# Performance work log

Hardware: AMD Instinct MI355X
Metric: run time of the kernel (lower is better)

Reference implementation:

```python
import math
import jax, jax.numpy as jnp
import numpy as np

B, S, D, QK, H = 4, 4096, 1024, 128, 2048  # hidden = int(2.0 * dim)
NUM_BUCKETS, MAX_DIST = 32, 128
LN_EPS = 1e-5


def setup_inputs() -> dict:
    key = jax.random.key(0)
    ks = jax.random.split(key, 7)
    x = jax.random.normal(ks[0], (B, S, D), jnp.float32)
    ln_g = jnp.ones((D,), jnp.float32)
    ln_b = jnp.zeros((D,), jnp.float32)
    Wh = jax.random.normal(ks[1], (D, 2 * H), jnp.float32) * 0.02
    bh = jnp.zeros((2 * H,), jnp.float32)
    Wqk = jax.random.normal(ks[2], (D, QK), jnp.float32) * 0.02
    bqk = jnp.zeros((QK,), jnp.float32)
    os_gamma = jax.random.normal(ks[3], (2, QK), jnp.float32) * 0.02  # nn.init.normal_(std=0.02)
    os_beta = jnp.zeros((2, QK), jnp.float32)
    Wo = jax.random.normal(ks[4], (H, D), jnp.float32) * 0.02
    bo = jnp.zeros((D,), jnp.float32)
    rel_emb = jax.random.normal(ks[5], (NUM_BUCKETS, 1), jnp.float32) * 0.02
    return {"x": x, "ln_g": ln_g, "ln_b": ln_b, "Wh": Wh, "bh": bh,
            "Wqk": Wqk, "bqk": bqk, "os_gamma": os_gamma, "os_beta": os_beta,
            "Wo": Wo, "bo": bo, "rel_emb": rel_emb}


def _t5_rel_bias(rel_emb, seq_len, scale):
    # non-causal T5 relative position bucket (num_buckets halved to 16)
    pos = jnp.arange(seq_len)
    rel = pos[None, :] - pos[:, None]  # k_pos - q_pos -> [i, j]
    n = -rel
    nb = NUM_BUCKETS // 2  # 16
    me = nb // 2           # max_exact = 8
    ret = (n < 0).astype(jnp.int32) * nb
    na = jnp.abs(n)
    val_large = me + (jnp.log(jnp.maximum(na, 1).astype(jnp.float32) / me)
                      / math.log(MAX_DIST / me) * (nb - me)).astype(jnp.int32)
    val_large = jnp.minimum(val_large, nb - 1)
    bucket = ret + jnp.where(na < me, na, val_large)  # [S, S] in [0, 31]
    return rel_emb[bucket, 0] * scale  # [S, S]


def reference(x, ln_g, ln_b, Wh, bh, Wqk, bqk, os_gamma, os_beta, Wo, bo, rel_emb):
    seq_len = x.shape[-2]
    # LayerNorm
    mu = jnp.mean(x, axis=-1, keepdims=True)
    var = jnp.mean(jnp.square(x - mu), axis=-1, keepdims=True)
    normed = (x - mu) * jax.lax.rsqrt(var + LN_EPS) * ln_g + ln_b
    # hidden (v, gate) with SiLU
    hidden = jax.nn.silu(normed @ Wh + bh)  # [B, S, 2H]
    v, gate = hidden[..., :H], hidden[..., H:]
    # qk projection + offset/scale into q, k
    qk = jax.nn.silu(normed @ Wqk + bqk)  # [B, S, QK]
    q = qk * os_gamma[0] + os_beta[0]
    k = qk * os_gamma[1] + os_beta[1]
    sim = jnp.einsum('bid,bjd->bij', q, k)  # [B, S, S]
    sim = sim + _t5_rel_bias(rel_emb, seq_len, float(D) ** 0.5)
    attn = jnp.square(jax.nn.relu(sim / seq_len))  # ReLU^2, no softmax
    out = jnp.einsum('bij,bjd->bid', attn, v) * gate  # [B, S, H]
    out = out @ Wo + bo
    return out + x  # add_residual
```

## Files before the change

### kernel.cpp

```cpp
#include <hip/hip_runtime.h>
#include <hip/hip_bf16.h>
#include <math.h>

typedef __bf16 bf16_t;
typedef __bf16 bf16x8 __attribute__((ext_vector_type(8)));
typedef __bf16 bf16x4 __attribute__((ext_vector_type(4)));
typedef float  f32x4  __attribute__((ext_vector_type(4)));
typedef int    i32x4  __attribute__((ext_vector_type(4)));

#define S_LEN 4096
#define D_DIM 1024
#define QK_DIM 128
#define H_DIM 2048
#define BATCH 4

__device__ __forceinline__ void gld_lds16(const void* g, void* l) {
  __builtin_amdgcn_global_load_lds((const __attribute__((address_space(1))) void*)g,
                                   (__attribute__((address_space(3))) void*)l, 16, 0, 0);
}

__device__ __forceinline__ float silu_f(float v) {
  return v / (1.0f + __expf(-v));
}

__device__ __forceinline__ bf16x8 as_bf(i32x4 v) {
  union { i32x4 a; bf16x8 b; } u; u.a = v; return u.b;
}

__device__ __forceinline__ float ldf(const void* p, size_t i, int f32) {
  return f32 ? ((const float*)p)[i] : (float)((const bf16_t*)p)[i];
}

__global__ void probe_k(const unsigned* __restrict__ ln_g_raw, int* __restrict__ flag) {
  if (threadIdx.x == 0) flag[0] = (ln_g_raw[0] == 0x3F800000u) ? 1 : 0;
}

#define M_HID 0
#define M_QK 1
#define M_SCORE 2
#define M_PV 3
#define M_OUT 4

template <int MODE, int K, int KS>
__global__ __launch_bounds__(512, (KS == 64 ? 2 : 4))
void gemm4(const bf16_t* __restrict__ A, const bf16_t* __restrict__ Bt,
           const void* e0, const void* e1, const float* __restrict__ ef,
           void* o0, void* o1, const int* __restrict__ dflag)
{
  constexpr int NT   = K / KS;
  constexpr int NSL  = KS / 32;
  constexpr int ASLOT = 128 * KS * 2;
  constexpr int BSLOT = 256 * KS * 2;
  constexpr int RA   = ASLOT / 8192;
  constexpr int RB   = BSLOT / 8192;
  constexpr int SLD  = RA + RB;
  constexpr int MR   = 4;
  constexpr int RWB  = KS * 2;

  __shared__ __align__(16) char lds[3 * (ASLOT + BSLOT)];

  const int t = threadIdx.x;
  const int w = t >> 6, lane = t & 63;
  const int quad = lane >> 4, col = lane & 15;
  const int wm = (w >> 2) * 64;
  const int wn = (w & 3) * 64;

  const int gx = gridDim.x;
  const int nwg = gx * (int)gridDim.y;
  const int orig = (int)blockIdx.y * gx + (int)blockIdx.x;
  const int wg = (orig & 7) * (nwg >> 3) + (orig >> 3);
  const int bx = wg & (gx - 1), by = wg >> __builtin_ctz(gx);
  const int m0 = bx * 128, n0 = by * 256;

  const bf16_t* const Ap = A + (size_t)m0 * K;
  const bf16_t* const Bp = Bt + (size_t)n0 * K;

  size_t aoff[RA], boff[RB];
#pragma unroll
  for (int c = 0; c < RA; ++c) {
    const int P = c * 8192 + t * 16;
    const int L = P ^ (((P >> 7) & (NSL == 1 ? 3 : 7)) << 4);
    aoff[c] = (size_t)(L / RWB) * K + ((L & (RWB - 1)) >> 1);
  }
#pragma unroll
  for (int c = 0; c < RB; ++c) {
    const int P = c * 8192 + t * 16;
    const int L = P ^ (((P >> 7) & (NSL == 1 ? 3 : 7)) << 4);
    boff[c] = (size_t)(L / RWB) * K + ((L & (RWB - 1)) >> 1);
  }

  const int xr = (NSL == 1) ? ((quad ^ ((col >> 1) & 3)) << 4)
                            : ((quad ^ (col & 7)) << 4);
  const unsigned ldsI = (unsigned)(size_t)&lds[0];
  const unsigned aStat = ldsI + (unsigned)((wm + col) * RWB + xr);
  const unsigned bStat = ldsI + 3u * ASLOT + (unsigned)((wn + col) * RWB + xr);

  f32x4 acc[MR][4] = {};
  i32x4 aF[MR][NSL], bF[4][NSL];

#define SB() __builtin_amdgcn_sched_barrier(0)
#define BARR() do { SB(); __builtin_amdgcn_s_barrier(); SB(); } while (0)
#define DSR(dst, addr, lit) \
  asm volatile("ds_read_b128 %0, %1 offset:" #lit : "=v"(dst) : "v"(addr))
#define WL(n) asm volatile("s_waitcnt lgkmcnt(" #n ")" ::: "memory")
#define WAITV0() asm volatile("s_waitcnt vmcnt(0)" ::: "memory")
#define VWS() do {                                                             \
    if constexpr (SLD == 3) asm volatile("s_waitcnt vmcnt(3)" ::: "memory");   \
    else                    asm volatile("s_waitcnt vmcnt(6)" ::: "memory");   \
  } while (0)

#define MMI(mi, ni, kk)                                                        \
  acc[mi][ni] = __builtin_amdgcn_mfma_f32_16x16x32_bf16(                       \
      as_bf(aF[mi][kk]), as_bf(bF[ni][kk]), acc[mi][ni], 0, 0, 0)
#define MM4(ni, kk) do { MMI(0, ni, kk); MMI(1, ni, kk);                       \
                         MMI(2, ni, kk); MMI(3, ni, kk); } while (0)

#define STG(ts, sl) do {                                                       \
    char* da_ = (char*)lds + (sl) * ASLOT + t * 16;                            \
    char* db_ = (char*)lds + 3 * ASLOT + (sl) * BSLOT + t * 16;                \
    const bf16_t* ga_ = Ap + (size_t)(ts) * KS;                                \
    const bf16_t* gb_ = Bp + (size_t)(ts) * KS;                                \
    _Pragma("unroll") for (int c_ = 0; c_ < RA; ++c_)                          \
      gld_lds16(ga_ + aoff[c_], da_ + c_ * 8192);                              \
    _Pragma("unroll") for (int c_ = 0; c_ < RB; ++c_)                          \
      gld_lds16(gb_ + boff[c_], db_ + c_ * 8192);                              \
  } while (0)

  STG(0, 0);
  STG(1, 1);
  VWS();
  BARR();

  int bsel = 0, ssel = 2;
  for (int tt = 0; tt < NT; ++tt) {
    const unsigned aAd = aStat + (unsigned)(bsel * ASLOT);
    const unsigned bAd = bStat + (unsigned)(bsel * BSLOT);
    if constexpr (NSL == 1) {
      DSR(bF[0][0], bAd, 0);
      DSR(aF[0][0], aAd, 0);
      DSR(aF[1][0], aAd, 1024);
      DSR(aF[2][0], aAd, 2048);
      DSR(aF[3][0], aAd, 3072);
      DSR(bF[1][0], bAd, 1024);
      DSR(bF[2][0], bAd, 2048);
      DSR(bF[3][0], bAd, 3072);
      if (tt + 2 < NT) STG(tt + 2, ssel);
      __builtin_amdgcn_s_setprio(1);
      WL(6); SB(); MMI(0, 0, 0);
      WL(5); SB(); MMI(1, 0, 0);
      WL(4); SB(); MMI(2, 0, 0);
      WL(3); SB(); MMI(3, 0, 0);
      WL(2); SB(); MM4(1, 0);
      WL(1); SB(); MM4(2, 0);
      WL(0); SB(); MM4(3, 0);
      __builtin_amdgcn_s_setprio(0);
    } else {
      const unsigned aA1 = aAd ^ 64u, bA1 = bAd ^ 64u;
      DSR(bF[0][0], bAd, 0);
      DSR(aF[0][0], aAd, 0);
      DSR(aF[1][0], aAd, 2048);
      DSR(aF[2][0], aAd, 4096);
      DSR(aF[3][0], aAd, 6144);
      DSR(bF[1][0], bAd, 2048);
      DSR(bF[2][0], bAd, 4096);
      DSR(bF[3][0], bAd, 6144);
      DSR(bF[0][1], bA1, 0);
      DSR(aF[0][1], aA1, 0);
      DSR(aF[1][1], aA1, 2048);
      DSR(aF[2][1], aA1, 4096);
      DSR(aF[3][1], aA1, 6144);
      DSR(bF[1][1], bA1, 2048);
      DSR(bF[2][1], bA1, 4096);
      DSR(bF[3][1], bA1, 6144);
      if (tt + 2 < NT) STG(tt + 2, ssel);
      __builtin_amdgcn_s_setprio(1);
      WL(14); SB(); MMI(0, 0, 0);
      WL(13); SB(); MMI(1, 0, 0);
      WL(12); SB(); MMI(2, 0, 0);
      WL(11); SB(); MMI(3, 0, 0);
      WL(10); SB(); MM4(1, 0);
      WL(9);  SB(); MM4(2, 0);
      WL(8);  SB(); MM4(3, 0);
      WL(6);  SB(); MMI(0, 0, 1);
      WL(5);  SB(); MMI(1, 0, 1);
      WL(4);  SB(); MMI(2, 0, 1);
      WL(3);  SB(); MMI(3, 0, 1);
      WL(2);  SB(); MM4(1, 1);
      WL(1);  SB(); MM4(2, 1);
      WL(0);  SB(); MM4(3, 1);
      __builtin_amdgcn_s_setprio(0);
    }
    SB();
    if (tt + 1 < NT) {
      if (tt + 2 < NT) VWS();
      else WAITV0();
    }
    BARR();
    bsel = (bsel == 2) ? 0 : bsel + 1;
    ssel = (ssel == 2) ? 0 : ssel + 1;
  }

#undef SB
#undef BARR
#undef DSR
#undef WL
#undef WAITV0
#undef VWS
#undef MMI
#undef MM4
#undef STG

  __syncthreads();

  int f32 = 0;
  if constexpr (MODE == M_HID || MODE == M_OUT) f32 = dflag[0];

  if constexpr (MODE == M_OUT) {
    float (*swzf)[16][68] = (float (*)[16][68])lds;
#pragma unroll
    for (int m = 0; m < MR; ++m) {
      __syncthreads();
#pragma unroll
      for (int j = 0; j < 4; ++j)
#pragma unroll
        for (int r = 0; r < 4; ++r)
          swzf[w][quad * 4 + r][j * 16 + col] = acc[m][j][r];
      __syncthreads();
#pragma unroll
      for (int it = 0; it < 4; ++it) {
        const int task = it * 64 + lane, gr = task >> 4, ch = task & 15;
        const int gm = m0 + wm + m * 16 + gr;
        const int gnc = n0 + wn + ch * 4;
        f32x4 vv = *(const f32x4*)&swzf[w][gr][ch * 4];
        float xr4[4], r4[4];
        if (f32) {
          float4 t4 = *(const float4*)((const float*)e1 + (size_t)gm * D_DIM + gnc);
          xr4[0] = t4.x; xr4[1] = t4.y; xr4[2] = t4.z; xr4[3] = t4.w;
        } else {
          bf16x4 t4 = *(const bf16x4*)((const bf16_t*)e1 + (size_t)gm * D_DIM + gnc);
#pragma unroll
          for (int qq = 0; qq < 4; ++qq) xr4[qq] = (float)t4[qq];
        }
#pragma unroll
        for (int qq = 0; qq < 4; ++qq)
          r4[qq] = vv[qq] + ldf(e0, gnc + qq, f32) + xr4[qq];
        if (f32) {
          float4 s4 = {r4[0], r4[1], r4[2], r4[3]};
          *(float4*)((float*)o0 + (size_t)gm * D_DIM + gnc) = s4;
        } else {
          bf16x4 s4;
#pragma unroll
          for (int qq = 0; qq < 4; ++qq) s4[qq] = (bf16_t)r4[qq];
          *(bf16x4*)((bf16_t*)o0 + (size_t)gm * D_DIM + gnc) = s4;
        }
      }
    }
    return;
  }

  if constexpr (MODE == M_HID) {
    if (n0 < H_DIM) {
      bf16_t (*swzT)[16][72] = (bf16_t (*)[16][72])lds;
      const int bb  = m0 >> 12;
      const int smb = (m0 + wm) & (S_LEN - 1);
#pragma unroll
      for (int j = 0; j < 4; ++j) {
        __syncthreads();
        const int gnj = n0 + wn + j * 16;
        const float bhv = ldf(e0, gnj + col, f32);
#pragma unroll
        for (int m = 0; m < MR; ++m)
#pragma unroll
          for (int r = 0; r < 4; ++r)
            swzT[w][col][m * 16 + quad * 4 + r] = (bf16_t)silu_f(acc[m][j][r] + bhv);
        __syncthreads();
#pragma unroll
        for (int it = 0; it < 2; ++it) {
          const int task = it * 64 + lane, gr = task >> 3, ch = task & 7;
          bf16x8 vv = *(const bf16x8*)&swzT[w][gr][ch * 8];
          const size_t off = ((size_t)bb * H_DIM + (gnj + gr)) * S_LEN + smb + ch * 8;
          *(bf16x8*)((bf16_t*)o0 + off) = vv;
        }
      }
      return;
    }
  }

  if constexpr (MODE == M_HID || MODE == M_SCORE || MODE == M_PV) {
    bf16_t (*swzb)[16][72] = (bf16_t (*)[16][72])lds;
#pragma unroll
    for (int m = 0; m < MR; ++m) {
      __syncthreads();
#pragma unroll
      for (int j = 0; j < 4; ++j) {
        const int gn = n0 + wn + j * 16 + col;
#pragma unroll
        for (int r = 0; r < 4; ++r) {
          const float val = acc[m][j][r];
          bf16_t sv;
          if constexpr (MODE == M_HID) {
            sv = (bf16_t)silu_f(val + ldf(e0, gn, f32));
          } else if constexpr (MODE == M_SCORE) {
            const int gm = m0 + wm + m * 16 + quad * 4 + r;
            float wgt = fmaxf((val + ef[gm - gn + (S_LEN - 1)]) *
                              (1.0f / (float)S_LEN), 0.0f);
            sv = (bf16_t)(wgt * wgt);
          } else {
            sv = (bf16_t)val;
          }
          swzb[w][quad * 4 + r][j * 16 + col] = sv;
        }
      }
      __syncthreads();
#pragma unroll
      for (int it = 0; it < 2; ++it) {
        const int task = it * 64 + lane, gr = task >> 3, ch = task & 7;
        const int gm  = m0 + wm + m * 16 + gr;
        const int gnb = n0 + wn + ch * 8;
        bf16x8 vv = *(const bf16x8*)&swzb[w][gr][ch * 8];
        if constexpr (MODE == M_HID) {
          *(bf16x8*)((bf16_t*)o1 + (size_t)gm * H_DIM + (gnb - H_DIM)) = vv;
        } else if constexpr (MODE == M_SCORE) {
          *(bf16x8*)((bf16_t*)o0 + (size_t)gm * S_LEN + gnb) = vv;
        } else {
          bf16x8 g8 = *(const bf16x8*)((const bf16_t*)e0 + (size_t)gm * H_DIM + gnb);
          bf16x8 r8;
#pragma unroll
          for (int qq = 0; qq < 8; ++qq)
            r8[qq] = (bf16_t)((float)vv[qq] * (float)g8[qq]);
          *(bf16x8*)((bf16_t*)o0 + (size_t)gm * H_DIM + gnb) = r8;
        }
      }
    }
  }
}

template <int MODE>
__global__ __launch_bounds__(256)
void gemm_bt(const bf16_t* __restrict__ A, const bf16_t* __restrict__ Bt,
             int M, int N, int K,
             const void* e0, const void* e1, const void* e2,
             const float* __restrict__ ef,
             void* o0, void* o1, const int* __restrict__ dflag)
{
  __shared__ __align__(16) bf16_t As[128 * 32];
  __shared__ __align__(16) bf16_t Bs[128 * 32];
  const int t = threadIdx.x;
  const int w = t >> 6, lane = t & 63;
  const int quad = lane >> 4, col = lane & 15;
  const int wm = (w >> 1) << 6, wn = (w & 1) << 6;
  const int m0 = blockIdx.x * 128, n0 = blockIdx.y * 128;
  const int f32 = dflag[0];

  f32x4 acc[4][4] = {};

  for (int k0 = 0; k0 < K; k0 += 32) {
    __syncthreads();
    for (int p = 0; p < 2; ++p) {
      const int chunk = w * 2 + p;
      const int fl = (chunk * 64 + lane) * 8;
      const int r = fl >> 5, c = fl & 31;
      gld_lds16(A  + (size_t)(m0 + r) * K + (k0 + c), &As[chunk * 512]);
      gld_lds16(Bt + (size_t)(n0 + r) * K + (k0 + c), &Bs[chunk * 512]);
    }
    __syncthreads();

    bf16x8 af[4], bfr[4];
#pragma unroll
    for (int i = 0; i < 4; ++i)
      af[i] = *(const bf16x8*)&As[(wm + i * 16 + col) * 32 + quad * 8];
#pragma unroll
    for (int i = 0; i < 4; ++i)
      bfr[i] = *(const bf16x8*)&Bs[(wn + i * 16 + col) * 32 + quad * 8];
#pragma unroll
    for (int i = 0; i < 4; ++i)
#pragma unroll
      for (int j = 0; j < 4; ++j)
        acc[i][j] = __builtin_amdgcn_mfma_f32_16x16x32_bf16(af[i], bfr[j], acc[i][j], 0, 0, 0);
  }

#pragma unroll
  for (int i = 0; i < 4; ++i) {
#pragma unroll
    for (int j = 0; j < 4; ++j) {
#pragma unroll
      for (int r = 0; r < 4; ++r) {
        const int gm = m0 + wm + i * 16 + quad * 4 + r;
        const int gn = n0 + wn + j * 16 + col;
        float val = acc[i][j][r] + ldf(e0, gn, f32);
        float s = silu_f(val);
        ((bf16_t*)o0)[(size_t)gm * QK_DIM + gn] =
            (bf16_t)(s * ldf(e1, gn, f32) + ldf(e2, gn, f32));
        ((bf16_t*)o1)[(size_t)gm * QK_DIM + gn] =
            (bf16_t)(s * ldf(e1, QK_DIM + gn, f32) + ldf(e2, QK_DIM + gn, f32));
      }
    }
  }
}

__global__ __launch_bounds__(256)
void layernorm_k(const void* __restrict__ x, const void* __restrict__ g,
                 const void* __restrict__ be, bf16_t* __restrict__ out,
                 const int* __restrict__ dflag)
{
  const int row = blockIdx.x;
  const int t = threadIdx.x;
  const int f32 = dflag[0];
  float f[4];
  if (f32) {
    const float* xr = (const float*)x + (size_t)row * D_DIM;
    float4 xv = *(const float4*)&xr[t * 4];
    f[0] = xv.x; f[1] = xv.y; f[2] = xv.z; f[3] = xv.w;
  } else {
    const bf16_t* xr = (const bf16_t*)x + (size_t)row * D_DIM;
    bf16x4 xv = *(const bf16x4*)&xr[t * 4];
#pragma unroll
    for (int i = 0; i < 4; ++i) f[i] = (float)xv[i];
  }
  float s = 0.f, sq = 0.f;
#pragma unroll
  for (int i = 0; i < 4; ++i) { s += f[i]; sq += f[i] * f[i]; }
#pragma unroll
  for (int off = 32; off > 0; off >>= 1) {
    s += __shfl_down(s, off);
    sq += __shfl_down(sq, off);
  }
  __shared__ float red[8];
  const int w = t >> 6;
  if ((t & 63) == 0) { red[w] = s; red[4 + w] = sq; }
  __syncthreads();
  s = red[0] + red[1] + red[2] + red[3];
  sq = red[4] + red[5] + red[6] + red[7];
  const float mu = s * (1.0f / D_DIM);
  const float var = sq * (1.0f / D_DIM) - mu * mu;
  const float inv = rsqrtf(var + 1e-5f);
  bf16x4 ov;
#pragma unroll
  for (int i = 0; i < 4; ++i) {
    float nv = (f[i] - mu) * inv * ldf(g, t * 4 + i, f32) + ldf(be, t * 4 + i, f32);
    ov[i] = (bf16_t)nv;
  }
  *(bf16x4*)&out[(size_t)row * D_DIM + t * 4] = ov;
}

__global__ __launch_bounds__(256)
void transpose_k(const void* __restrict__ src, bf16_t* __restrict__ dst,
                 int R, int C, const int* __restrict__ dflag)
{
  __shared__ bf16_t tile[32][33];
  const int f32 = dflag[0];
  const int c0 = blockIdx.x * 32, r0 = blockIdx.y * 32;
  for (int i = threadIdx.y; i < 32; i += 8)
    tile[i][threadIdx.x] = (bf16_t)ldf(src, (size_t)(r0 + i) * C + (c0 + threadIdx.x), f32);
  __syncthreads();
  for (int i = threadIdx.y; i < 32; i += 8)
    dst[(size_t)(c0 + i) * R + (r0 + threadIdx.x)] = tile[threadIdx.x][i];
}

__global__ void bias_k(const void* __restrict__ rel_emb, float* __restrict__ bias,
                       const int* __restrict__ dflag)
{
  int d = blockIdx.x * 256 + threadIdx.x;
  if (d >= 2 * S_LEN - 1) return;
  const int f32 = dflag[0];
  int n = d - (S_LEN - 1);
  int ret = (n < 0) ? 16 : 0;
  int na = n < 0 ? -n : n;
  int b;
  if (na < 8) b = na;
  else {
    float vl = logf((float)na * (1.0f / 8.0f)) / logf(16.0f) * 8.0f;
    int vi = 8 + (int)vl;
    b = vi > 15 ? 15 : vi;
  }
  bias[d] = ldf(rel_emb, ret + b, f32) * 32.0f;
}

extern "C" void kernel_launch(void* const* d_in, const int* in_sizes, int n_in,
                              void* d_out, int out_size, void* d_ws, size_t ws_size,
                              hipStream_t stream)
{
  const void* x    = d_in[0];
  const void* ln_g = d_in[1];
  const void* ln_b = d_in[2];
  const void* Wh   = d_in[3];
  const void* bh   = d_in[4];
  const void* Wqk  = d_in[5];
  const void* bqk  = d_in[6];
  const void* osg  = d_in[7];
  const void* osb  = d_in[8];
  const void* Wo   = d_in[9];
  const void* bo   = d_in[10];
  const void* rel  = d_in[11];

  const int BS = BATCH * S_LEN;
  char* p = (char*)d_ws;
  int*    flags  = (int*)p;     p += 256;
  float*  bias   = (float*)p;   p += (size_t)8192 * 4;
  bf16_t* WhT    = (bf16_t*)p;  p += (size_t)4096 * 1024 * 2;
  bf16_t* WqkT   = (bf16_t*)p;  p += (size_t)128 * 1024 * 2;
  bf16_t* WoT    = (bf16_t*)p;  p += (size_t)1024 * 2048 * 2;
  bf16_t* q      = (bf16_t*)p;  p += (size_t)BS * QK_DIM * 2;
  bf16_t* kk     = (bf16_t*)p;  p += (size_t)BS * QK_DIM * 2;
  bf16_t* vT     = (bf16_t*)p;  p += (size_t)BS * H_DIM * 2;
  bf16_t* gate   = (bf16_t*)p;  p += (size_t)BS * H_DIM * 2;
  bf16_t* normed = (bf16_t*)p;  p += (size_t)BS * D_DIM * 2;
  bf16_t* attn   = normed;
  bf16_t* pvg    = gate;

  probe_k<<<1, 64, 0, stream>>>((const unsigned*)ln_g, flags);
  bias_k<<<32, 256, 0, stream>>>(rel, bias, flags);
  transpose_k<<<dim3(4096 / 32, 1024 / 32), dim3(32, 8), 0, stream>>>(Wh, WhT, 1024, 4096, flags);
  transpose_k<<<dim3(128 / 32, 1024 / 32), dim3(32, 8), 0, stream>>>(Wqk, WqkT, 1024, 128, flags);
  transpose_k<<<dim3(1024 / 32, 2048 / 32), dim3(32, 8), 0, stream>>>(Wo, WoT, 2048, 1024, flags);
  layernorm_k<<<BS, 256, 0, stream>>>(x, ln_g, ln_b, normed, flags);

  gemm4<M_HID, 1024, 32><<<dim3(BS / 128, 4096 / 256), 512, 0, stream>>>(
      normed, WhT, bh, nullptr, nullptr, vT, gate, flags);
  gemm_bt<M_QK><<<dim3(BS / 128, 1), 256, 0, stream>>>(
      normed, WqkT, BS, QK_DIM, 1024, bqk, osg, osb, nullptr, q, kk, flags);

  for (int b = 0; b < BATCH; ++b) {
    gemm4<M_SCORE, QK_DIM, 32><<<dim3(S_LEN / 128, S_LEN / 256), 512, 0, stream>>>(
        q + (size_t)b * S_LEN * QK_DIM, kk + (size_t)b * S_LEN * QK_DIM,
        nullptr, nullptr, bias, attn, nullptr, flags);
    gemm4<M_PV, S_LEN, 64><<<dim3(S_LEN / 128, H_DIM / 256), 512, 0, stream>>>(
        attn, vT + (size_t)b * S_LEN * H_DIM,
        gate + (size_t)b * S_LEN * H_DIM, nullptr, nullptr,
        pvg + (size_t)b * S_LEN * H_DIM, nullptr, flags);
  }

  gemm4<M_OUT, H_DIM, 32><<<dim3(BS / 128, 1024 / 256), 512, 0, stream>>>(
      pvg, WoT, bo, x, nullptr, d_out, nullptr, flags);
}
```

Baseline: 770.0 us.

## Load A operand directly from global into registers, bypassing LDS staging

Removes LDS staging for the A tile in the shared GEMM kernel; each wave now issues global_load_dwordx4 for its A fragments one k-step ahead into a register double buffer, while B stays on the LDS pipeline. This cuts LDS footprint and ds_read traffic for A. In exchange, A rows are fetched redundantly by multiple waves with less coalesced access, and register pressure rises from the extra fragment buffer.

```diff
diff --git a/kernel.cpp b/kernel.cpp
--- a/kernel.cpp
+++ b/kernel.cpp
@@ -43,21 +43,17 @@
 
 template <int MODE, int K, int KS>
 __global__ __launch_bounds__(512, (KS == 64 ? 2 : 4))
-void gemm4(const bf16_t* __restrict__ A, const bf16_t* __restrict__ Bt,
+void gemm5(const bf16_t* __restrict__ A, const bf16_t* __restrict__ Bt,
            const void* e0, const void* e1, const float* __restrict__ ef,
            void* o0, void* o1, const int* __restrict__ dflag)
 {
   constexpr int NT   = K / KS;
   constexpr int NSL  = KS / 32;
-  constexpr int ASLOT = 128 * KS * 2;
   constexpr int BSLOT = 256 * KS * 2;
-  constexpr int RA   = ASLOT / 8192;
   constexpr int RB   = BSLOT / 8192;
-  constexpr int SLD  = RA + RB;
-  constexpr int MR   = 4;
   constexpr int RWB  = KS * 2;
 
-  __shared__ __align__(16) char lds[3 * (ASLOT + BSLOT)];
+  __shared__ __align__(16) char lds[3 * BSLOT];
 
   const int t = threadIdx.x;
   const int w = t >> 6, lane = t & 63;
@@ -75,13 +71,7 @@
   const bf16_t* const Ap = A + (size_t)m0 * K;
   const bf16_t* const Bp = Bt + (size_t)n0 * K;
 
-  size_t aoff[RA], boff[RB];
-#pragma unroll
-  for (int c = 0; c < RA; ++c) {
-    const int P = c * 8192 + t * 16;
-    const int L = P ^ (((P >> 7) & (NSL == 1 ? 3 : 7)) << 4);
-    aoff[c] = (size_t)(L / RWB) * K + ((L & (RWB - 1)) >> 1);
-  }
+  size_t boff[RB];
 #pragma unroll
   for (int c = 0; c < RB; ++c) {
     const int P = c * 8192 + t * 16;
@@ -92,40 +82,61 @@
   const int xr = (NSL == 1) ? ((quad ^ ((col >> 1) & 3)) << 4)
                             : ((quad ^ (col & 7)) << 4);
   const unsigned ldsI = (unsigned)(size_t)&lds[0];
-  const unsigned aStat = ldsI + (unsigned)((wm + col) * RWB + xr);
-  const unsigned bStat = ldsI + 3u * ASLOT + (unsigned)((wn + col) * RWB + xr);
-
-  f32x4 acc[MR][4] = {};
-  i32x4 aF[MR][NSL], bF[4][NSL];
+  const unsigned bStat = ldsI + (unsigned)((wn + col) * RWB + xr);
+
+  unsigned voff[4];
+#pragma unroll
+  for (int mi = 0; mi < 4; ++mi)
+    voff[mi] = (unsigned)(((wm + mi * 16 + col) * (size_t)K + quad * 8) * 2);
+
+  f32x4 acc[4][4] = {};
+  i32x4 aCur[4][NSL], aNxt[4][NSL], bF[4][NSL];
 
 #define SB() __builtin_amdgcn_sched_barrier(0)
 #define BARR() do { SB(); __builtin_amdgcn_s_barrier(); SB(); } while (0)
 #define DSR(dst, addr, lit) \
   asm volatile("ds_read_b128 %0, %1 offset:" #lit : "=v"(dst) : "v"(addr))
+#define GLA(dst, off, lit) \
+  asm volatile("global_load_dwordx4 %0, %1, %2 offset:" #lit \
+               : "=v"(dst) : "v"(off), "s"(Ap))
 #define WL(n) asm volatile("s_waitcnt lgkmcnt(" #n ")" ::: "memory")
 #define WAITV0() asm volatile("s_waitcnt vmcnt(0)" ::: "memory")
 #define VWS() do {                                                             \
-    if constexpr (SLD == 3) asm volatile("s_waitcnt vmcnt(3)" ::: "memory");   \
-    else                    asm volatile("s_waitcnt vmcnt(6)" ::: "memory");   \
+    if constexpr (RB == 2) asm volatile("s_waitcnt vmcnt(2)" ::: "memory");    \
+    else                   asm volatile("s_waitcnt vmcnt(4)" ::: "memory");    \
+  } while (0)
+
+#define LDA(dst) do {                                                          \
+    _Pragma("unroll") for (int mi_ = 0; mi_ < 4; ++mi_) {                      \
+      GLA(dst[mi_][0], voff[mi_], 0);                                          \
+      if constexpr (NSL == 2) GLA(dst[mi_][1], voff[mi_], 64);                 \
+    }                                                                          \
+  } while (0)
+
+#define ACOPY() do {                                                           \
+    _Pragma("unroll") for (int mi_ = 0; mi_ < 4; ++mi_)                        \
+    _Pragma("unroll") for (int kk_ = 0; kk_ < NSL; ++kk_)                      \
+      aCur[mi_][kk_] = aNxt[mi_][kk_];                                         \
+    _Pragma("unroll") for (int mi_ = 0; mi_ < 4; ++mi_)                        \
+      voff[mi_] += KS * 2;                                                     \
   } while (0)
 
 #define MMI(mi, ni, kk)                                                        \
   acc[mi][ni] = __builtin_amdgcn_mfma_f32_16x16x32_bf16(                       \
-      as_bf(aF[mi][kk]), as_bf(bF[ni][kk]), acc[mi][ni], 0, 0, 0)
+      as_bf(aCur[mi][kk]), as_bf(bF[ni][kk]), acc[mi][ni], 0, 0, 0)
 #define MM4(ni, kk) do { MMI(0, ni, kk); MMI(1, ni, kk);                       \
                          MMI(2, ni, kk); MMI(3, ni, kk); } while (0)
 
 #define STG(ts, sl) do {                                                       \
-    char* da_ = (char*)lds + (sl) * ASLOT + t * 16;                            \
-    char* db_ = (char*)lds + 3 * ASLOT + (sl) * BSLOT + t * 16;                \
-    const bf16_t* ga_ = Ap + (size_t)(ts) * KS;                                \
+    char* db_ = (char*)lds + (sl) * BSLOT + t * 16;                            \
     const bf16_t* gb_ = Bp + (size_t)(ts) * KS;                                \
-    _Pragma("unroll") for (int c_ = 0; c_ < RA; ++c_)                          \
-      gld_lds16(ga_ + aoff[c_], da_ + c_ * 8192);                              \
     _Pragma("unroll") for (int c_ = 0; c_ < RB; ++c_)                          \
       gld_lds16(gb_ + boff[c_], db_ + c_ * 8192);                              \
   } while (0)
 
+  LDA(aCur);
+#pragma unroll
+  for (int mi = 0; mi < 4; ++mi) voff[mi] += KS * 2;
   STG(0, 0);
   STG(1, 1);
   VWS();
@@ -133,69 +144,49 @@
 
   int bsel = 0, ssel = 2;
   for (int tt = 0; tt < NT; ++tt) {
-    const unsigned aAd = aStat + (unsigned)(bsel * ASLOT);
     const unsigned bAd = bStat + (unsigned)(bsel * BSLOT);
     if constexpr (NSL == 1) {
       DSR(bF[0][0], bAd, 0);
-      DSR(aF[0][0], aAd, 0);
-      DSR(aF[1][0], aAd, 1024);
-      DSR(aF[2][0], aAd, 2048);
-      DSR(aF[3][0], aAd, 3072);
       DSR(bF[1][0], bAd, 1024);
       DSR(bF[2][0], bAd, 2048);
       DSR(bF[3][0], bAd, 3072);
-      if (tt + 2 < NT) STG(tt + 2, ssel);
-      __builtin_amdgcn_s_setprio(1);
-      WL(6); SB(); MMI(0, 0, 0);
-      WL(5); SB(); MMI(1, 0, 0);
-      WL(4); SB(); MMI(2, 0, 0);
-      WL(3); SB(); MMI(3, 0, 0);
-      WL(2); SB(); MM4(1, 0);
-      WL(1); SB(); MM4(2, 0);
-      WL(0); SB(); MM4(3, 0);
-      __builtin_amdgcn_s_setprio(0);
     } else {
-      const unsigned aA1 = aAd ^ 64u, bA1 = bAd ^ 64u;
+      const unsigned bA1 = bAd ^ 64u;
       DSR(bF[0][0], bAd, 0);
-      DSR(aF[0][0], aAd, 0);
-      DSR(aF[1][0], aAd, 2048);
-      DSR(aF[2][0], aAd, 4096);
-      DSR(aF[3][0], aAd, 6144);
       DSR(bF[1][0], bAd, 2048);
       DSR(bF[2][0], bAd, 4096);
       DSR(bF[3][0], bAd, 6144);
       DSR(bF[0][1], bA1, 0);
-      DSR(aF[0][1], aA1, 0);
-      DSR(aF[1][1], aA1, 2048);
-      DSR(aF[2][1], aA1, 4096);
-      DSR(aF[3][1], aA1, 6144);
       DSR(bF[1][1], bA1, 2048);
       DSR(bF[2][1], bA1, 4096);
       DSR(bF[3][1], bA1, 6144);
-      if (tt + 2 < NT) STG(tt + 2, ssel);
-      __builtin_amdgcn_s_setprio(1);
-      WL(14); SB(); MMI(0, 0, 0);
-      WL(13); SB(); MMI(1, 0, 0);
-      WL(12); SB(); MMI(2, 0, 0);
-      WL(11); SB(); MMI(3, 0, 0);
-      WL(10); SB(); MM4(1, 0);
-      WL(9);  SB(); MM4(2, 0);
-      WL(8);  SB(); MM4(3, 0);
-      WL(6);  SB(); MMI(0, 0, 1);
-      WL(5);  SB(); MMI(1, 0, 1);
-      WL(4);  SB(); MMI(2, 0, 1);
-      WL(3);  SB(); MMI(3, 0, 1);
-      WL(2);  SB(); MM4(1, 1);
-      WL(1);  SB(); MM4(2, 1);
-      WL(0);  SB(); MM4(3, 1);
-      __builtin_amdgcn_s_setprio(0);
-    }
+    }
+    if (tt + 1 < NT) LDA(aNxt);
+    if (tt + 2 < NT) STG(tt + 2, ssel);
+    __builtin_amdgcn_s_setprio(1);
+    if constexpr (NSL == 1) {
+      WL(3); SB(); MM4(0, 0);
+      WL(2); SB(); MM4(1, 0);
+      WL(1); SB(); MM4(2, 0);
+      WL(0); SB(); MM4(3, 0);
+    } else {
+      WL(7); SB(); MM4(0, 0);
+      WL(6); SB(); MM4(1, 0);
+      WL(5); SB(); MM4(2, 0);
+      WL(4); SB(); MM4(3, 0);
+      WL(3); SB(); MM4(0, 1);
+      WL(2); SB(); MM4(1, 1);
+      WL(1); SB(); MM4(2, 1);
+      WL(0); SB(); MM4(3, 1);
+    }
+    __builtin_amdgcn_s_setprio(0);
     SB();
     if (tt + 1 < NT) {
       if (tt + 2 < NT) VWS();
       else WAITV0();
     }
     BARR();
+    if (tt + 1 < NT) ACOPY();
     bsel = (bsel == 2) ? 0 : bsel + 1;
     ssel = (ssel == 2) ? 0 : ssel + 1;
   }
@@ -203,9 +194,12 @@
 #undef SB
 #undef BARR
 #undef DSR
+#undef GLA
 #undef WL
 #undef WAITV0
 #undef VWS
+#undef LDA
+#undef ACOPY
 #undef MMI
 #undef MM4
 #undef STG
@@ -218,7 +212,7 @@
   if constexpr (MODE == M_OUT) {
     float (*swzf)[16][68] = (float (*)[16][68])lds;
 #pragma unroll
-    for (int m = 0; m < MR; ++m) {
+    for (int m = 0; m < 4; ++m) {
       __syncthreads();
 #pragma unroll
       for (int j = 0; j < 4; ++j)
@@ -269,7 +263,7 @@
         const int gnj = n0 + wn + j * 16;
         const float bhv = ldf(e0, gnj + col, f32);
 #pragma unroll
-        for (int m = 0; m < MR; ++m)
+        for (int m = 0; m < 4; ++m)
 #pragma unroll
           for (int r = 0; r < 4; ++r)
             swzT[w][col][m * 16 + quad * 4 + r] = (bf16_t)silu_f(acc[m][j][r] + bhv);
@@ -289,7 +283,7 @@
   if constexpr (MODE == M_HID || MODE == M_SCORE || MODE == M_PV) {
     bf16_t (*swzb)[16][72] = (bf16_t (*)[16][72])lds;
 #pragma unroll
-    for (int m = 0; m < MR; ++m) {
+    for (int m = 0; m < 4; ++m) {
       __syncthreads();
 #pragma unroll
       for (int j = 0; j < 4; ++j) {
@@ -515,21 +509,21 @@
   transpose_k<<<dim3(1024 / 32, 2048 / 32), dim3(32, 8), 0, stream>>>(Wo, WoT, 2048, 1024, flags);
   layernorm_k<<<BS, 256, 0, stream>>>(x, ln_g, ln_b, normed, flags);
 
-  gemm4<M_HID, 1024, 32><<<dim3(BS / 128, 4096 / 256), 512, 0, stream>>>(
+  gemm5<M_HID, 1024, 32><<<dim3(BS / 128, 4096 / 256), 512, 0, stream>>>(
       normed, WhT, bh, nullptr, nullptr, vT, gate, flags);
   gemm_bt<M_QK><<<dim3(BS / 128, 1), 256, 0, stream>>>(
       normed, WqkT, BS, QK_DIM, 1024, bqk, osg, osb, nullptr, q, kk, flags);
 
   for (int b = 0; b < BATCH; ++b) {
-    gemm4<M_SCORE, QK_DIM, 32><<<dim3(S_LEN / 128, S_LEN / 256), 512, 0, stream>>>(
+    gemm5<M_SCORE, QK_DIM, 32><<<dim3(S_LEN / 128, S_LEN / 256), 512, 0, stream>>>(
         q + (size_t)b * S_LEN * QK_DIM, kk + (size_t)b * S_LEN * QK_DIM,
         nullptr, nullptr, bias, attn, nullptr, flags);
-    gemm4<M_PV, S_LEN, 64><<<dim3(S_LEN / 128, H_DIM / 256), 512, 0, stream>>>(
+    gemm5<M_PV, S_LEN, 64><<<dim3(S_LEN / 128, H_DIM / 256), 512, 0, stream>>>(
         attn, vT + (size_t)b * S_LEN * H_DIM,
         gate + (size_t)b * S_LEN * H_DIM, nullptr, nullptr,
         pvg + (size_t)b * S_LEN * H_DIM, nullptr, flags);
   }
 
-  gemm4<M_OUT, H_DIM, 32><<<dim3(BS / 128, 1024 / 256), 512, 0, stream>>>(
+  gemm5<M_OUT, H_DIM, 32><<<dim3(BS / 128, 1024 / 256), 512, 0, stream>>>(
       pvg, WoT, bo, x, nullptr, d_out, nullptr, flags);
 }
```

After: 1.428 ms. 1.85x slower.
